# Kernel tuning notes

Hardware: AMD Instinct MI355X
Metric: run time of the kernel (lower is better)

Reference implementation:

```python
import jax, jax.numpy as jnp
import numpy as np
from functools import partial

# Block hyperparams (match init_kwargs)
B, C, N, H = 16, 512, 1024, 8
HID = 4 * C
TAU, THRESH, SG_SCALE = 2.0, 1.0, 5.0
ATTN_SCALE = 0.25
BN_EPS = 1e-5

# LIF spiking neuron (single-step, stateless): membrane v = x / tau, hard threshold
# forward; sigmoid surrogate gradient (scale=5.0) in backward.
@partial(jax.custom_vjp, nondiff_argnums=(1,))
def spike(u, scale):
    return (u >= 0.0).astype(u.dtype)

def _spike_fwd(u, scale):
    return spike(u, scale), u

def _spike_bwd(scale, u, g):
    s = jax.nn.sigmoid(scale * u)
    return (g * scale * s * (1.0 - s),)

spike.defvjp(_spike_fwd, _spike_bwd)

def lif(x):
    return spike(x / TAU - THRESH, SG_SCALE)

def conv1x1(x, w, b=None):
    # x: [B,C,N], w: [O,C] -> [B,O,N]
    y = jnp.einsum('oc,bcn->bon', w, x)
    return y if b is None else y + b[None, :, None]

def bn(x, g, b):
    # BatchNorm1d, training-mode batch stats over (batch, length), biased var
    m = jnp.mean(x, axis=(0, 2), keepdims=True)
    v = jnp.var(x, axis=(0, 2), keepdims=True)
    return (x - m) * jax.lax.rsqrt(v + BN_EPS) * g[None, :, None] + b[None, :, None]


def setup_inputs() -> dict:
    key = jax.random.key(0)
    ks = jax.random.split(key, 8)
    w = lambda k, o, i: jax.random.normal(k, (o, i), dtype=jnp.float32) * 0.02
    inp = {
        'x': jax.random.normal(ks[0], (B, C, N), dtype=jnp.float32),
        'q_w': w(ks[1], C, C), 'q_g': jnp.ones((C,), jnp.float32), 'q_b': jnp.zeros((C,), jnp.float32),
        'k_w': w(ks[2], C, C), 'k_g': jnp.ones((C,), jnp.float32), 'k_b': jnp.zeros((C,), jnp.float32),
        'v_w': w(ks[3], C, C), 'v_g': jnp.ones((C,), jnp.float32), 'v_b': jnp.zeros((C,), jnp.float32),
        'proj_w': w(ks[4], C, C), 'proj_bias': jnp.zeros((C,), jnp.float32),
        'proj_g': jnp.ones((C,), jnp.float32), 'proj_b': jnp.zeros((C,), jnp.float32),
        'fc1_w': w(ks[5], HID, C), 'fc1_bias': jnp.zeros((HID,), jnp.float32),
        'fc1_g': jnp.ones((HID,), jnp.float32), 'fc1_b': jnp.zeros((HID,), jnp.float32),
        'fc2_w': w(ks[6], C, HID), 'fc2_bias': jnp.zeros((C,), jnp.float32),
        'fc2_g': jnp.ones((C,), jnp.float32), 'fc2_b': jnp.zeros((C,), jnp.float32),
    }
    return inp


def reference(x, q_w, q_g, q_b, k_w, k_g, k_b, v_w, v_g, v_b,
              proj_w, proj_bias, proj_g, proj_b,
              fc1_w, fc1_bias, fc1_g, fc1_b, fc2_w, fc2_bias, fc2_g, fc2_b):
    Bb, Cc, Nn = x.shape
    D = Cc // H

    def heads(t):  # [B,C,N] -> [B,H,N,D]
        return t.transpose(0, 2, 1).reshape(Bb, Nn, H, D).transpose(0, 2, 1, 3)

    # spiking attention (no softmax): (Q K^T) V * 0.25
    q = heads(lif(bn(conv1x1(x, q_w), q_g, q_b)))
    k = heads(lif(bn(conv1x1(x, k_w), k_g, k_b)))
    v = heads(lif(bn(conv1x1(x, v_w), v_g, v_b)))
    scores = jnp.einsum('bhnd,bhmd->bhnm', q, k)            # [B,H,N,N]
    attn = jnp.einsum('bhnm,bhmd->bhnd', scores, v) * ATTN_SCALE
    a = attn.transpose(0, 1, 3, 2).reshape(Bb, Cc, Nn)       # [B,C,N]
    a = lif(a)
    a = lif(bn(conv1x1(a, proj_w, proj_bias), proj_g, proj_b))
    x = x + a                                                # residual 1

    # conv1x1-BN-LIF MLP
    h = lif(bn(conv1x1(x, fc1_w, fc1_bias), fc1_g, fc1_b))
    h = lif(bn(conv1x1(h, fc2_w, fc2_bias), fc2_g, fc2_b))
    return x + h                                             # residual 2
```

## Files before the change

kernel.cpp:

```cpp
#include <hip/hip_runtime.h>
#include <stdint.h>

#pragma clang fp contract(off)

#define BATCH 16
#define CCH   512
#define NLEN  1024
#define NH    8
#define DH    64

__device__ float pw128(const float* __restrict__ x) {
    float r0=x[0],r1=x[1],r2=x[2],r3=x[3],r4=x[4],r5=x[5],r6=x[6],r7=x[7];
    for (int i = 8; i < 128; i += 8) {
        r0 += x[i+0]; r1 += x[i+1]; r2 += x[i+2]; r3 += x[i+3];
        r4 += x[i+4]; r5 += x[i+5]; r6 += x[i+6]; r7 += x[i+7];
    }
    return ((r0+r1)+(r2+r3))+((r4+r5)+(r6+r7));
}
__device__ float pw128_sqdev(const float* __restrict__ x, float m) {
    float r0,r1,r2,r3,r4,r5,r6,r7;
    {
        float d;
        d = x[0]-m; r0 = d*d;  d = x[1]-m; r1 = d*d;
        d = x[2]-m; r2 = d*d;  d = x[3]-m; r3 = d*d;
        d = x[4]-m; r4 = d*d;  d = x[5]-m; r5 = d*d;
        d = x[6]-m; r6 = d*d;  d = x[7]-m; r7 = d*d;
    }
    for (int i = 8; i < 128; i += 8) {
        float d;
        d = x[i+0]-m; r0 += d*d;  d = x[i+1]-m; r1 += d*d;
        d = x[i+2]-m; r2 += d*d;  d = x[i+3]-m; r3 += d*d;
        d = x[i+4]-m; r4 += d*d;  d = x[i+5]-m; r5 += d*d;
        d = x[i+6]-m; r6 += d*d;  d = x[i+7]-m; r7 += d*d;
    }
    return ((r0+r1)+(r2+r3))+((r4+r5)+(r6+r7));
}

__global__ __launch_bounds__(64) void bn_stats_np_k(const float* __restrict__ Y, int O,
                                                    float2* __restrict__ st)
{
    const int o = blockIdx.x;
    const int t = threadIdx.x;
    const int bi = t >> 2, q = t & 3;
    __shared__ float part[64];
    __shared__ float msh;
    const float* p = Y + ((size_t)bi * O + o) * NLEN + q * 256;
    {
        float s0 = pw128(p), s1 = pw128(p + 128);
        part[t] = s0 + s1;
    }
    __syncthreads();
    if (t == 0) {
        float s = 0.0f;
        for (int b = 0; b < 16; ++b) {
            const float* pp = &part[b * 4];
            float v = (pp[0] + pp[1]) + (pp[2] + pp[3]);
            s = (b == 0) ? v : (s + v);
        }
        msh = s / 16384.0f;
    }
    __syncthreads();
    const float m = msh;
    {
        float s0 = pw128_sqdev(p, m), s1 = pw128_sqdev(p + 128, m);
        part[t] = s0 + s1;
    }
    __syncthreads();
    if (t == 0) {
        float s = 0.0f;
        for (int b = 0; b < 16; ++b) {
            const float* pp = &part[b * 4];
            float v = (pp[0] + pp[1]) + (pp[2] + pp[3]);
            s = (b == 0) ? v : (s + v);
        }
        float var = s / 16384.0f;
        float ve  = var + 1e-5f;
        float sq  = (float)sqrt((double)ve);
        float r   = (float)(1.0 / (double)sq);
        st[o] = make_float2(m, r);
    }
}

__device__ inline bool spike_f32(float y, float2 s, float g, float b) {
    float t1 = y - s.x;
    float t2 = t1 * s.y;
    float t3 = t2 * g;
    float t4 = t3 + b;
    float u  = t4 / 2.0f - 1.0f;
    return u >= 0.0f;
}

template<int MODE>
__global__ __launch_bounds__(256) void gemm_k(
    const float* __restrict__ W, const float* __restrict__ Xf, const uint8_t* __restrict__ Xs8,
    const float* __restrict__ bias, float* __restrict__ Y,
    int O, int Cin, int N)
{
    __shared__ float Ws[2][16][132];
    __shared__ float Xs[2][16][132];
    const int b = blockIdx.z;
    const size_t xbase = (size_t)b * Cin * N;
    float* Yb = Y + (size_t)b * O * N;
    const int o0 = blockIdx.y * 128;
    const int n0 = blockIdx.x * 128;
    const int t  = threadIdx.x;
    const int tx = t & 15;
    const int ty = t >> 4;

    const int wr = t >> 1;
    const int wk = (t & 1) << 3;
    const int xk = t >> 4;
    const int xc = (t & 15) << 3;

    float acc[8][8];
#pragma unroll
    for (int i = 0; i < 8; ++i)
#pragma unroll
        for (int j = 0; j < 8; ++j) acc[i][j] = 0.0f;

    float4 wA[2];
    float  xr[8];

    auto loadG = [&](int k0) {
        const float* wp = W + (size_t)(o0 + wr) * Cin + k0 + wk;
        wA[0] = *reinterpret_cast<const float4*>(wp);
        wA[1] = *reinterpret_cast<const float4*>(wp + 4);
        size_t off = xbase + (size_t)(k0 + xk) * N + n0 + xc;
        float4 v0 = *reinterpret_cast<const float4*>(Xf + off);
        float4 v1 = *reinterpret_cast<const float4*>(Xf + off + 4);
        if (MODE == 0) {
            xr[0]=v0.x; xr[1]=v0.y; xr[2]=v0.z; xr[3]=v0.w;
            xr[4]=v1.x; xr[5]=v1.y; xr[6]=v1.z; xr[7]=v1.w;
        } else {
            uchar4 u0 = *reinterpret_cast<const uchar4*>(Xs8 + off);
            uchar4 u1 = *reinterpret_cast<const uchar4*>(Xs8 + off + 4);
            xr[0]=v0.x+(float)u0.x; xr[1]=v0.y+(float)u0.y;
            xr[2]=v0.z+(float)u0.z; xr[3]=v0.w+(float)u0.w;
            xr[4]=v1.x+(float)u1.x; xr[5]=v1.y+(float)u1.y;
            xr[6]=v1.z+(float)u1.z; xr[7]=v1.w+(float)u1.w;
        }
    };
    auto stage = [&](int buf) {
        Ws[buf][wk+0][wr]=wA[0].x; Ws[buf][wk+1][wr]=wA[0].y;
        Ws[buf][wk+2][wr]=wA[0].z; Ws[buf][wk+3][wr]=wA[0].w;
        Ws[buf][wk+4][wr]=wA[1].x; Ws[buf][wk+5][wr]=wA[1].y;
        Ws[buf][wk+6][wr]=wA[1].z; Ws[buf][wk+7][wr]=wA[1].w;
        *reinterpret_cast<float4*>(&Xs[buf][xk][xc])     = make_float4(xr[0],xr[1],xr[2],xr[3]);
        *reinterpret_cast<float4*>(&Xs[buf][xk][xc + 4]) = make_float4(xr[4],xr[5],xr[6],xr[7]);
    };

    loadG(0);
    stage(0);
    __syncthreads();
    int cur = 0;
    for (int k0 = 0;;) {
        const int kn = k0 + 16;
        const bool more = kn < Cin;
        if (more) loadG(kn);
#pragma unroll
        for (int kk = 0; kk < 16; ++kk) {
            float4 a0 = *reinterpret_cast<const float4*>(&Ws[cur][kk][ty * 4]);
            float4 a1 = *reinterpret_cast<const float4*>(&Ws[cur][kk][64 + ty * 4]);
            float4 b0 = *reinterpret_cast<const float4*>(&Xs[cur][kk][tx * 4]);
            float4 b1 = *reinterpret_cast<const float4*>(&Xs[cur][kk][64 + tx * 4]);
            float av[8] = {a0.x,a0.y,a0.z,a0.w,a1.x,a1.y,a1.z,a1.w};
            float bv[8] = {b0.x,b0.y,b0.z,b0.w,b1.x,b1.y,b1.z,b1.w};
#pragma unroll
            for (int i = 0; i < 8; ++i)
#pragma unroll
                for (int j = 0; j < 8; ++j)
                    acc[i][j] = fmaf(av[i], bv[j], acc[i][j]);
        }
        if (!more) break;
        stage(cur ^ 1);
        __syncthreads();
        cur ^= 1;
        k0 = kn;
    }
#pragma unroll
    for (int half = 0; half < 2; ++half)
#pragma unroll
        for (int i = 0; i < 4; ++i) {
            const int r = half * 4 + i;
            const int o = o0 + half * 64 + ty * 4 + i;
            const float bb = bias ? bias[o] : 0.0f;
            float* yp = Yb + (size_t)o * N + n0;
            float4 r0, r1;
            r0.x = acc[r][0] + bb; r0.y = acc[r][1] + bb;
            r0.z = acc[r][2] + bb; r0.w = acc[r][3] + bb;
            r1.x = acc[r][4] + bb; r1.y = acc[r][5] + bb;
            r1.z = acc[r][6] + bb; r1.w = acc[r][7] + bb;
            *reinterpret_cast<float4*>(yp + tx * 4)      = r0;
            *reinterpret_cast<float4*>(yp + 64 + tx * 4) = r1;
        }
}

__global__ __launch_bounds__(256) void wt_k(const float* __restrict__ W, float* __restrict__ Wt,
                                            int O, int Cin)
{
    __shared__ float tile[32][33];
    const int k0 = blockIdx.x * 32, o0 = blockIdx.y * 32;
    const int tx = threadIdx.x & 31, ty = threadIdx.x >> 5;
#pragma unroll
    for (int j = 0; j < 4; ++j)
        tile[ty + 8*j][tx] = W[(size_t)(o0 + ty + 8*j) * Cin + k0 + tx];
    __syncthreads();
#pragma unroll
    for (int j = 0; j < 4; ++j)
        Wt[(size_t)(k0 + ty + 8*j) * O + o0 + tx] = tile[tx][ty + 8*j];
}

__global__ __launch_bounds__(256) void col_bits_k(const uint8_t* __restrict__ S,
                                                  unsigned long long* __restrict__ bits, int Cin)
{
    const int n0 = blockIdx.x * 64, kw = blockIdx.y, b = blockIdx.z;
    __shared__ uint8_t tile[64][64];
    const int t = threadIdx.x;
    const int r = t >> 2, cg = (t & 3) * 16;
    const uint8_t* src = S + ((size_t)b * Cin + kw * 64 + r) * NLEN + n0 + cg;
    *reinterpret_cast<uint4*>(&tile[r][cg]) = *reinterpret_cast<const uint4*>(src);
    __syncthreads();
    if (t < 64) {
        unsigned long long m = 0;
#pragma unroll
        for (int rr = 0; rr < 64; ++rr)
            m |= ((unsigned long long)(tile[rr][t] != 0)) << rr;
        bits[((size_t)b * NLEN + n0 + t) * (Cin >> 6) + kw] = m;
    }
}

__global__ __launch_bounds__(256) void sparse_gemm_k(
    const float* __restrict__ Wt, const unsigned long long* __restrict__ bits,
    const float* __restrict__ bias, float* __restrict__ Y, int Cin)
{
    const int wid  = (blockIdx.x << 2) + (threadIdx.x >> 6);
    const int lane = threadIdx.x & 63;
    const int b = wid >> 10, n = wid & 1023;
    const int W64 = Cin >> 6;
    float acc[8];
#pragma unroll
    for (int i = 0; i < 8; ++i) acc[i] = 0.0f;
    const unsigned long long* bp = bits + ((size_t)b * NLEN + n) * W64;
    for (int w = 0; w < W64; ++w) {
        unsigned long long m = bp[w];
        while (m) {
            const int bit = __builtin_ctzll(m);
            m &= m - 1;
            const int k = (w << 6) + bit;
            const float* wr = Wt + ((size_t)k << 9) + lane * 8;
            float4 w0 = *reinterpret_cast<const float4*>(wr);
            float4 w1 = *reinterpret_cast<const float4*>(wr + 4);
            acc[0] += w0.x; acc[1] += w0.y; acc[2] += w0.z; acc[3] += w0.w;
            acc[4] += w1.x; acc[5] += w1.y; acc[6] += w1.z; acc[7] += w1.w;
        }
    }
    const float* bq = bias + lane * 8;
    float4 b0 = *reinterpret_cast<const float4*>(bq);
    float4 b1 = *reinterpret_cast<const float4*>(bq + 4);
    float bi[8] = {b0.x, b0.y, b0.z, b0.w, b1.x, b1.y, b1.z, b1.w};
    float* yp = Y + ((size_t)b * 512 + lane * 8) * NLEN + n;
#pragma unroll
    for (int i = 0; i < 8; ++i)
        yp[(size_t)i * NLEN] = acc[i] + bi[i];
}

__global__ __launch_bounds__(256) void spike_pack_qkv_k(
    const float* __restrict__ Y, const float2* __restrict__ st,
    const float* __restrict__ gq, const float* __restrict__ gk, const float* __restrict__ gv,
    const float* __restrict__ bq, const float* __restrict__ bk, const float* __restrict__ bv,
    uint8_t* __restrict__ oq, uint8_t* __restrict__ ok, uint8_t* __restrict__ ov)
{
    const int nt = blockIdx.x, hs = blockIdx.y, b = blockIdx.z;
    const int tensor = hs >> 3, h = hs & 7;
    const float* g  = (tensor == 0) ? gq : (tensor == 1) ? gk : gv;
    const float* be = (tensor == 0) ? bq : (tensor == 1) ? bk : bv;
    uint8_t* outp   = (tensor == 0) ? oq : (tensor == 1) ? ok : ov;
    __shared__ uint8_t tile[64][68];
    const int t = threadIdx.x;
    {
        const int i = t & 63, dq = t >> 6;
#pragma unroll
        for (int p = 0; p < 16; ++p) {
            int d  = dq * 16 + p;
            int cf = hs * 64 + d;
            int cl = h * 64 + d;
            float y = Y[((size_t)b * 1536 + cf) * NLEN + nt * 64 + i];
            tile[d][i] = spike_f32(y, st[cf], g[cl], be[cl]) ? 1 : 0;
        }
    }
    __syncthreads();
    {
        const int d = t & 63, iq = t >> 6;
#pragma unroll
        for (int p = 0; p < 16; ++p) {
            int i = iq * 16 + p;
            outp[((size_t)(b * NH + h) * NLEN + nt * 64 + i) * DH + d] = tile[d][i];
        }
    }
}

__global__ __launch_bounds__(256) void ktv_k(const uint8_t* __restrict__ Kb, const uint8_t* __restrict__ Vb,
                                             float* __restrict__ M)
{
    const int bh = blockIdx.x;
    const uint8_t* kp = Kb + (size_t)bh * NLEN * DH;
    const uint8_t* vp = Vb + (size_t)bh * NLEN * DH;
    __shared__ float ks[64][68];
    __shared__ float vs[64][68];
    const int t = threadIdx.x;
    const int d2 = t & 63, g4 = t >> 6;
    float acc[16];
#pragma unroll
    for (int j = 0; j < 16; ++j) acc[j] = 0.f;

    for (int nc = 0; nc < NLEN; nc += 64) {
#pragma unroll
        for (int p = 0; p < 16; ++p) {
            int idx = t + p * 256;
            int r = idx >> 6, d = idx & 63;
            ks[r][d] = (float)kp[(size_t)(nc + r) * DH + d];
            vs[r][d] = (float)vp[(size_t)(nc + r) * DH + d];
        }
        __syncthreads();
        for (int n = 0; n < 64; ++n) {
            float vv = vs[n][d2];
#pragma unroll
            for (int j = 0; j < 16; ++j)
                acc[j] += ks[n][g4 * 16 + j] * vv;
        }
        __syncthreads();
    }
#pragma unroll
    for (int j = 0; j < 16; ++j)
        M[(size_t)bh * 4096 + (size_t)(g4 * 16 + j) * 64 + d2] = acc[j];
}

__global__ __launch_bounds__(256) void attn_spike_k(const uint8_t* __restrict__ Qb, const float* __restrict__ M,
                                                    uint8_t* __restrict__ A)
{
    const int nt = blockIdx.x, h = blockIdx.y, b = blockIdx.z;
    const int bh = b * NH + h;
    __shared__ float Ms[64][68];
    __shared__ float qs[64][65];
    const int t = threadIdx.x;
#pragma unroll
    for (int p = 0; p < 16; ++p) {
        int idx = t + p * 256;
        int r = idx >> 6, c = idx & 63;
        Ms[r][c] = M[(size_t)bh * 4096 + idx];
        qs[c][r] = (float)Qb[((size_t)bh * NLEN + nt * 64 + r) * DH + c];
    }
    __syncthreads();
    const int n = t & 63, dg = t >> 6;
    float acc[16];
#pragma unroll
    for (int j = 0; j < 16; ++j) acc[j] = 0.f;
    for (int d1 = 0; d1 < 64; ++d1) {
        float qv = qs[d1][n];
#pragma unroll
        for (int j = 0; j < 16; ++j)
            acc[j] += qv * Ms[d1][dg * 16 + j];
    }
#pragma unroll
    for (int j = 0; j < 16; ++j) {
        int d = dg * 16 + j;
        A[((size_t)b * CCH + h * 64 + d) * NLEN + nt * 64 + n] = (acc[j] >= 8.0f) ? 1 : 0;
    }
}

__global__ __launch_bounds__(256) void spike_store_k(
    const float* __restrict__ Y, const float2* __restrict__ st,
    const float* __restrict__ g, const float* __restrict__ bet,
    uint8_t* __restrict__ H, int Oc, int o_off, int Otot)
{
    size_t i4 = (size_t)blockIdx.x * 256 + threadIdx.x;
    size_t total = (size_t)BATCH * Oc * (NLEN / 4);
    if (i4 >= total) return;
    int n4 = (int)(i4 & 255);
    int o  = (int)((i4 >> 8) % Oc);
    int b  = (int)(i4 / ((size_t)256 * Oc));
    float4 y = reinterpret_cast<const float4*>(Y)[i4];
    float2 s = st[o];
    float gg = g[o], bb = bet[o];
    uchar4 r;
    r.x = spike_f32(y.x, s, gg, bb) ? 1 : 0;
    r.y = spike_f32(y.y, s, gg, bb) ? 1 : 0;
    r.z = spike_f32(y.z, s, gg, bb) ? 1 : 0;
    r.w = spike_f32(y.w, s, gg, bb) ? 1 : 0;
    *reinterpret_cast<uchar4*>(H + ((size_t)(b * Otot + o_off + o)) * NLEN + n4 * 4) = r;
}

__global__ __launch_bounds__(256) void final_k(
    const float* __restrict__ Y, const float2* __restrict__ st,
    const float* __restrict__ g, const float* __restrict__ bet,
    const float* __restrict__ x, const uint8_t* __restrict__ ares,
    float* __restrict__ Out)
{
    size_t i4 = (size_t)blockIdx.x * 256 + threadIdx.x;
    size_t total = (size_t)BATCH * CCH * (NLEN / 4);
    if (i4 >= total) return;
    int o = (int)((i4 >> 8) % CCH);
    float4 y  = reinterpret_cast<const float4*>(Y)[i4];
    float4 xv = reinterpret_cast<const float4*>(x)[i4];
    uchar4 av = reinterpret_cast<const uchar4*>(ares)[i4];
    float2 s = st[o];
    float gg = g[o], bb = bet[o];
    float4 r;
    {
        float x1;
        x1 = xv.x + (float)av.x; r.x = x1 + (spike_f32(y.x, s, gg, bb) ? 1.0f : 0.0f);
        x1 = xv.y + (float)av.y; r.y = x1 + (spike_f32(y.y, s, gg, bb) ? 1.0f : 0.0f);
        x1 = xv.z + (float)av.z; r.z = x1 + (spike_f32(y.z, s, gg, bb) ? 1.0f : 0.0f);
        x1 = xv.w + (float)av.w; r.w = x1 + (spike_f32(y.w, s, gg, bb) ? 1.0f : 0.0f);
    }
    reinterpret_cast<float4*>(Out)[i4] = r;
}

extern "C" void kernel_launch(void* const* d_in, const int* in_sizes, int n_in,
                              void* d_out, int out_size, void* d_ws, size_t ws_size,
                              hipStream_t stream)
{
    const float* x         = (const float*)d_in[0];
    const float* q_w       = (const float*)d_in[1];
    const float* q_g       = (const float*)d_in[2];
    const float* q_b       = (const float*)d_in[3];
    const float* k_w       = (const float*)d_in[4];
    const float* k_g       = (const float*)d_in[5];
    const float* k_b       = (const float*)d_in[6];
    const float* v_w       = (const float*)d_in[7];
    const float* v_g       = (const float*)d_in[8];
    const float* v_b       = (const float*)d_in[9];
    const float* proj_w    = (const float*)d_in[10];
    const float* proj_bias = (const float*)d_in[11];
    const float* proj_g    = (const float*)d_in[12];
    const float* proj_b    = (const float*)d_in[13];
    const float* fc1_w     = (const float*)d_in[14];
    const float* fc1_bias  = (const float*)d_in[15];
    const float* fc1_g     = (const float*)d_in[16];
    const float* fc1_b     = (const float*)d_in[17];
    const float* fc2_w     = (const float*)d_in[18];
    const float* fc2_bias  = (const float*)d_in[19];
    const float* fc2_g     = (const float*)d_in[20];
    const float* fc2_b     = (const float*)d_in[21];
    float* out = (float*)d_out;

    char* ws = (char*)d_ws;
    const size_t MiB = 1ull << 20;
    if (ws_size < 124 * MiB) return;

    float*    Yq    = (float*)(ws);
    float*    Af    = (float*)(ws);
    uint8_t*  ab    = (uint8_t*)(ws);
    uint8_t*  ares  = (uint8_t*)(ws + 64 * MiB);
    uint8_t*  hb    = (uint8_t*)(ws + 72 * MiB);
    uint8_t*  qb    = (uint8_t*)(ws + 96 * MiB);
    uint8_t*  kb    = (uint8_t*)(ws + 104 * MiB);
    uint8_t*  vb    = (uint8_t*)(ws + 112 * MiB);
    float*    Wt    = (float*)(ws + 104 * MiB);
    unsigned long long* bits = (unsigned long long*)(ws + 108 * MiB);
    float*    Wcat  = (float*)(ws + 120 * MiB);
    float*    Mbuf  = (float*)(ws + 120 * MiB);
    float2*   stats = (float2*)(ws + 123 * MiB);

    dim3 thr256(256);

    hipMemcpyAsync(Wcat,          q_w, (size_t)512 * 512 * 4, hipMemcpyDeviceToDevice, stream);
    hipMemcpyAsync(Wcat + 262144, k_w, (size_t)512 * 512 * 4, hipMemcpyDeviceToDevice, stream);
    hipMemcpyAsync(Wcat + 524288, v_w, (size_t)512 * 512 * 4, hipMemcpyDeviceToDevice, stream);
    gemm_k<0><<<dim3(8, 12, 16), thr256, 0, stream>>>(Wcat, x, nullptr, nullptr, Yq, 1536, 512, 1024);
    bn_stats_np_k<<<dim3(1536), dim3(64), 0, stream>>>(Yq, 1536, stats);
    spike_pack_qkv_k<<<dim3(16, 24, 16), thr256, 0, stream>>>(Yq, stats, q_g, k_g, v_g,
                                                              q_b, k_b, v_b, qb, kb, vb);

    ktv_k<<<dim3(128), thr256, 0, stream>>>(kb, vb, Mbuf);
    attn_spike_k<<<dim3(16, 8, 16), thr256, 0, stream>>>(qb, Mbuf, ab);

    wt_k<<<dim3(16, 16), thr256, 0, stream>>>(proj_w, Wt, 512, 512);
    col_bits_k<<<dim3(16, 8, 16), thr256, 0, stream>>>(ab, bits, 512);
    sparse_gemm_k<<<dim3(4096), thr256, 0, stream>>>(Wt, bits, proj_bias, Af, 512);
    bn_stats_np_k<<<dim3(512), dim3(64), 0, stream>>>(Af, 512, stats);
    spike_store_k<<<dim3(8192), thr256, 0, stream>>>(Af, stats, proj_g, proj_b, ares, 512, 0, 512);

    for (int ch = 0; ch < 2; ++ch) {
        gemm_k<2><<<dim3(8, 8, 16), thr256, 0, stream>>>(fc1_w + (size_t)ch * 1024 * 512, x, ares,
                                                         fc1_bias + ch * 1024, Af, 1024, 512, 1024);
        bn_stats_np_k<<<dim3(1024), dim3(64), 0, stream>>>(Af, 1024, stats);
        spike_store_k<<<dim3(16384), thr256, 0, stream>>>(Af, stats, fc1_g + ch * 1024, fc1_b + ch * 1024,
                                                          hb, 1024, ch * 1024, 2048);
    }

    wt_k<<<dim3(64, 16), thr256, 0, stream>>>(fc2_w, Wt, 512, 2048);
    col_bits_k<<<dim3(16, 32, 16), thr256, 0, stream>>>(hb, bits, 2048);
    sparse_gemm_k<<<dim3(4096), thr256, 0, stream>>>(Wt, bits, fc2_bias, Af, 2048);
    bn_stats_np_k<<<dim3(512), dim3(64), 0, stream>>>(Af, 512, stats);
    final_k<<<dim3(8192), thr256, 0, stream>>>(Af, stats, fc2_g, fc2_b, x, ares, out);
}
```

Baseline: 1.450 ms.

## Split KtV across chunks, widen BN stats blocks, drop weight concat copies

The K^T V product is split into 8 sequence chunks per (batch, head) with a separate reduction kernel, which raises block count from 128 to 1024. BN statistics now use 128 threads per channel with a two-level shared reduction. The QKV GEMM picks its weight pointer per block instead of needing three device-to-device copies into a concatenated buffer. The spike-pack output stores and the attention/KtV shared-memory loads are vectorised. The costs are an extra partial-sum buffer and an extra launch, and the BN reduction order changes slightly.

```diff
diff --git a/kernel.cpp b/kernel.cpp
--- a/kernel.cpp
+++ b/kernel.cpp
@@ -36,24 +36,24 @@
     return ((r0+r1)+(r2+r3))+((r4+r5)+(r6+r7));
 }
 
-__global__ __launch_bounds__(64) void bn_stats_np_k(const float* __restrict__ Y, int O,
-                                                    float2* __restrict__ st)
+__global__ __launch_bounds__(128) void bn_stats_np_k(const float* __restrict__ Y, int O,
+                                                     float2* __restrict__ st)
 {
     const int o = blockIdx.x;
     const int t = threadIdx.x;
-    const int bi = t >> 2, q = t & 3;
-    __shared__ float part[64];
+    const int bi = t >> 3, h = t & 7;
+    __shared__ float part[128];
+    __shared__ float sq[64];
     __shared__ float msh;
-    const float* p = Y + ((size_t)bi * O + o) * NLEN + q * 256;
-    {
-        float s0 = pw128(p), s1 = pw128(p + 128);
-        part[t] = s0 + s1;
-    }
+    const float* p = Y + ((size_t)bi * O + o) * NLEN + h * 128;
+    part[t] = pw128(p);
+    __syncthreads();
+    if (t < 64) sq[t] = part[2 * t] + part[2 * t + 1];
     __syncthreads();
     if (t == 0) {
         float s = 0.0f;
         for (int b = 0; b < 16; ++b) {
-            const float* pp = &part[b * 4];
+            const float* pp = &sq[b * 4];
             float v = (pp[0] + pp[1]) + (pp[2] + pp[3]);
             s = (b == 0) ? v : (s + v);
         }
@@ -61,22 +61,21 @@
     }
     __syncthreads();
     const float m = msh;
-    {
-        float s0 = pw128_sqdev(p, m), s1 = pw128_sqdev(p + 128, m);
-        part[t] = s0 + s1;
-    }
+    part[t] = pw128_sqdev(p, m);
+    __syncthreads();
+    if (t < 64) sq[t] = part[2 * t] + part[2 * t + 1];
     __syncthreads();
     if (t == 0) {
         float s = 0.0f;
         for (int b = 0; b < 16; ++b) {
-            const float* pp = &part[b * 4];
+            const float* pp = &sq[b * 4];
             float v = (pp[0] + pp[1]) + (pp[2] + pp[3]);
             s = (b == 0) ? v : (s + v);
         }
         float var = s / 16384.0f;
         float ve  = var + 1e-5f;
-        float sq  = (float)sqrt((double)ve);
-        float r   = (float)(1.0 / (double)sq);
+        float sqv = (float)sqrt((double)ve);
+        float r   = (float)(1.0 / (double)sqv);
         st[o] = make_float2(m, r);
     }
 }
@@ -92,7 +91,8 @@
 
 template<int MODE>
 __global__ __launch_bounds__(256) void gemm_k(
-    const float* __restrict__ W, const float* __restrict__ Xf, const uint8_t* __restrict__ Xs8,
+    const float* __restrict__ Wq, const float* __restrict__ Wk, const float* __restrict__ Wv,
+    const float* __restrict__ Xf, const uint8_t* __restrict__ Xs8,
     const float* __restrict__ bias, float* __restrict__ Y,
     int O, int Cin, int N)
 {
@@ -101,7 +101,17 @@
     const int b = blockIdx.z;
     const size_t xbase = (size_t)b * Cin * N;
     float* Yb = Y + (size_t)b * O * N;
-    const int o0 = blockIdx.y * 128;
+    const int oy  = blockIdx.y;
+    const int o0y = oy * 128;
+    const float* W;
+    int o0w;
+    if (MODE == 0) {
+        W   = (oy < 4) ? Wq : (oy < 8) ? Wk : Wv;
+        o0w = (oy & 3) * 128;
+    } else {
+        W   = Wq;
+        o0w = o0y;
+    }
     const int n0 = blockIdx.x * 128;
     const int t  = threadIdx.x;
     const int tx = t & 15;
@@ -122,7 +132,7 @@
     float  xr[8];
 
     auto loadG = [&](int k0) {
-        const float* wp = W + (size_t)(o0 + wr) * Cin + k0 + wk;
+        const float* wp = W + (size_t)(o0w + wr) * Cin + k0 + wk;
         wA[0] = *reinterpret_cast<const float4*>(wp);
         wA[1] = *reinterpret_cast<const float4*>(wp + 4);
         size_t off = xbase + (size_t)(k0 + xk) * N + n0 + xc;
@@ -182,7 +192,7 @@
 #pragma unroll
         for (int i = 0; i < 4; ++i) {
             const int r = half * 4 + i;
-            const int o = o0 + half * 64 + ty * 4 + i;
+            const int o = o0y + half * 64 + ty * 4 + i;
             const float bb = bias ? bias[o] : 0.0f;
             float* yp = Yb + (size_t)o * N + n0;
             float4 r0, r1;
@@ -196,7 +206,7 @@
 }
 
 __global__ __launch_bounds__(256) void wt_k(const float* __restrict__ W, float* __restrict__ Wt,
-                                            int O, int Cin)
+                                            int O, int Cin, int o_off, int Otot)
 {
     __shared__ float tile[32][33];
     const int k0 = blockIdx.x * 32, o0 = blockIdx.y * 32;
@@ -207,7 +217,7 @@
     __syncthreads();
 #pragma unroll
     for (int j = 0; j < 4; ++j)
-        Wt[(size_t)(k0 + ty + 8*j) * O + o0 + tx] = tile[tx][ty + 8*j];
+        Wt[(size_t)(k0 + ty + 8*j) * Otot + o_off + o0 + tx] = tile[tx][ty + 8*j];
 }
 
 __global__ __launch_bounds__(256) void col_bits_k(const uint8_t* __restrict__ S,
@@ -290,49 +300,80 @@
     }
     __syncthreads();
     {
-        const int d = t & 63, iq = t >> 6;
-#pragma unroll
-        for (int p = 0; p < 16; ++p) {
-            int i = iq * 16 + p;
-            outp[((size_t)(b * NH + h) * NLEN + nt * 64 + i) * DH + d] = tile[d][i];
-        }
-    }
-}
-
-__global__ __launch_bounds__(256) void ktv_k(const uint8_t* __restrict__ Kb, const uint8_t* __restrict__ Vb,
-                                             float* __restrict__ M)
-{
-    const int bh = blockIdx.x;
+        const int d4 = (t & 15) * 4, ig = t >> 4;
+        uint8_t* ob = outp + ((size_t)(b * NH + h) * NLEN + nt * 64) * DH;
+#pragma unroll
+        for (int p = 0; p < 4; ++p) {
+            int i = p * 16 + ig;
+            uchar4 v;
+            v.x = tile[d4 + 0][i]; v.y = tile[d4 + 1][i];
+            v.z = tile[d4 + 2][i]; v.w = tile[d4 + 3][i];
+            *reinterpret_cast<uchar4*>(ob + (size_t)i * DH + d4) = v;
+        }
+    }
+}
+
+__global__ __launch_bounds__(256) void ktv_part_k(const uint8_t* __restrict__ Kb,
+                                                  const uint8_t* __restrict__ Vb,
+                                                  float* __restrict__ Mp)
+{
+    const int bh = blockIdx.x, ch = blockIdx.y;
     const uint8_t* kp = Kb + (size_t)bh * NLEN * DH;
     const uint8_t* vp = Vb + (size_t)bh * NLEN * DH;
     __shared__ float ks[64][68];
     __shared__ float vs[64][68];
     const int t = threadIdx.x;
     const int d2 = t & 63, g4 = t >> 6;
+    const int r2 = t >> 2, dq = (t & 3) * 16;
     float acc[16];
 #pragma unroll
     for (int j = 0; j < 16; ++j) acc[j] = 0.f;
 
-    for (int nc = 0; nc < NLEN; nc += 64) {
-#pragma unroll
-        for (int p = 0; p < 16; ++p) {
-            int idx = t + p * 256;
-            int r = idx >> 6, d = idx & 63;
-            ks[r][d] = (float)kp[(size_t)(nc + r) * DH + d];
-            vs[r][d] = (float)vp[(size_t)(nc + r) * DH + d];
+    for (int nc = ch * 128; nc < ch * 128 + 128; nc += 64) {
+        uint4 kv = *reinterpret_cast<const uint4*>(kp + (size_t)(nc + r2) * DH + dq);
+        uint4 vv = *reinterpret_cast<const uint4*>(vp + (size_t)(nc + r2) * DH + dq);
+        const uint8_t* k8 = reinterpret_cast<const uint8_t*>(&kv);
+        const uint8_t* v8 = reinterpret_cast<const uint8_t*>(&vv);
+#pragma unroll
+        for (int j = 0; j < 16; j += 4) {
+            float4 kf, vf;
+            kf.x = (float)k8[j+0]; kf.y = (float)k8[j+1];
+            kf.z = (float)k8[j+2]; kf.w = (float)k8[j+3];
+            vf.x = (float)v8[j+0]; vf.y = (float)v8[j+1];
+            vf.z = (float)v8[j+2]; vf.w = (float)v8[j+3];
+            *reinterpret_cast<float4*>(&ks[r2][dq + j]) = kf;
+            *reinterpret_cast<float4*>(&vs[r2][dq + j]) = vf;
         }
         __syncthreads();
         for (int n = 0; n < 64; ++n) {
-            float vv = vs[n][d2];
+            float vvv = vs[n][d2];
 #pragma unroll
             for (int j = 0; j < 16; ++j)
-                acc[j] += ks[n][g4 * 16 + j] * vv;
+                acc[j] += ks[n][g4 * 16 + j] * vvv;
         }
         __syncthreads();
     }
 #pragma unroll
     for (int j = 0; j < 16; ++j)
-        M[(size_t)bh * 4096 + (size_t)(g4 * 16 + j) * 64 + d2] = acc[j];
+        Mp[((size_t)ch * 128 + bh) * 4096 + (size_t)(g4 * 16 + j) * 64 + d2] = acc[j];
+}
+
+__global__ __launch_bounds__(256) void ktv_reduce_k(const float* __restrict__ Mp,
+                                                    float* __restrict__ M)
+{
+    const int bh = blockIdx.x;
+    const int t = threadIdx.x;
+#pragma unroll
+    for (int j = 0; j < 16; j += 4) {
+        const int idx = t * 16 + j;
+        float4 s = *reinterpret_cast<const float4*>(&Mp[(size_t)bh * 4096 + idx]);
+#pragma unroll
+        for (int c = 1; c < 8; ++c) {
+            float4 v = *reinterpret_cast<const float4*>(&Mp[((size_t)c * 128 + bh) * 4096 + idx]);
+            s.x += v.x; s.y += v.y; s.z += v.z; s.w += v.w;
+        }
+        *reinterpret_cast<float4*>(&M[(size_t)bh * 4096 + idx]) = s;
+    }
 }
 
 __global__ __launch_bounds__(256) void attn_spike_k(const uint8_t* __restrict__ Qb, const float* __restrict__ M,
@@ -343,12 +384,19 @@
     __shared__ float Ms[64][68];
     __shared__ float qs[64][65];
     const int t = threadIdx.x;
-#pragma unroll
-    for (int p = 0; p < 16; ++p) {
-        int idx = t + p * 256;
-        int r = idx >> 6, c = idx & 63;
-        Ms[r][c] = M[(size_t)bh * 4096 + idx];
-        qs[c][r] = (float)Qb[((size_t)bh * NLEN + nt * 64 + r) * DH + c];
+    const int r2 = t >> 2, cq = (t & 3) * 16;
+    {
+        const float* mp = M + (size_t)bh * 4096 + (size_t)r2 * 64 + cq;
+#pragma unroll
+        for (int u = 0; u < 4; ++u)
+            *reinterpret_cast<float4*>(&Ms[r2][cq + 4 * u]) =
+                *reinterpret_cast<const float4*>(mp + 4 * u);
+        uint4 qv = *reinterpret_cast<const uint4*>(
+            Qb + ((size_t)bh * NLEN + nt * 64 + r2) * DH + cq);
+        const uint8_t* q8 = reinterpret_cast<const uint8_t*>(&qv);
+#pragma unroll
+        for (int j = 0; j < 16; ++j)
+            qs[cq + j][r2] = (float)q8[j];
     }
     __syncthreads();
     const int n = t & 63, dg = t >> 6;
@@ -451,6 +499,7 @@
     float*    Yq    = (float*)(ws);
     float*    Af    = (float*)(ws);
     uint8_t*  ab    = (uint8_t*)(ws);
+    float*    Mpart = (float*)(ws + 16 * MiB);
     uint8_t*  ares  = (uint8_t*)(ws + 64 * MiB);
     uint8_t*  hb    = (uint8_t*)(ws + 72 * MiB);
     uint8_t*  qb    = (uint8_t*)(ws + 96 * MiB);
@@ -458,40 +507,40 @@
     uint8_t*  vb    = (uint8_t*)(ws + 112 * MiB);
     float*    Wt    = (float*)(ws + 104 * MiB);
     unsigned long long* bits = (unsigned long long*)(ws + 108 * MiB);
-    float*    Wcat  = (float*)(ws + 120 * MiB);
     float*    Mbuf  = (float*)(ws + 120 * MiB);
     float2*   stats = (float2*)(ws + 123 * MiB);
 
-    dim3 thr256(256);
-
-    hipMemcpyAsync(Wcat,          q_w, (size_t)512 * 512 * 4, hipMemcpyDeviceToDevice, stream);
-    hipMemcpyAsync(Wcat + 262144, k_w, (size_t)512 * 512 * 4, hipMemcpyDeviceToDevice, stream);
-    hipMemcpyAsync(Wcat + 524288, v_w, (size_t)512 * 512 * 4, hipMemcpyDeviceToDevice, stream);
-    gemm_k<0><<<dim3(8, 12, 16), thr256, 0, stream>>>(Wcat, x, nullptr, nullptr, Yq, 1536, 512, 1024);
-    bn_stats_np_k<<<dim3(1536), dim3(64), 0, stream>>>(Yq, 1536, stats);
+    dim3 thr256(256), thr128(128);
+
+    gemm_k<0><<<dim3(8, 12, 16), thr256, 0, stream>>>(q_w, k_w, v_w, x, nullptr, nullptr, Yq,
+                                                      1536, 512, 1024);
+    bn_stats_np_k<<<dim3(1536), thr128, 0, stream>>>(Yq, 1536, stats);
     spike_pack_qkv_k<<<dim3(16, 24, 16), thr256, 0, stream>>>(Yq, stats, q_g, k_g, v_g,
                                                               q_b, k_b, v_b, qb, kb, vb);
 
-    ktv_k<<<dim3(128), thr256, 0, stream>>>(kb, vb, Mbuf);
+    ktv_part_k<<<dim3(128, 8), thr256, 0, stream>>>(kb, vb, Mpart);
+    ktv_reduce_k<<<dim3(128), thr256, 0, stream>>>(Mpart, Mbuf);
     attn_spike_k<<<dim3(16, 8, 16), thr256, 0, stream>>>(qb, Mbuf, ab);
 
-    wt_k<<<dim3(16, 16), thr256, 0, stream>>>(proj_w, Wt, 512, 512);
+    wt_k<<<dim3(16, 16), thr256, 0, stream>>>(proj_w, Wt, 512, 512, 0, 512);
     col_bits_k<<<dim3(16, 8, 16), thr256, 0, stream>>>(ab, bits, 512);
     sparse_gemm_k<<<dim3(4096), thr256, 0, stream>>>(Wt, bits, proj_bias, Af, 512);
-    bn_stats_np_k<<<dim3(512), dim3(64), 0, stream>>>(Af, 512, stats);
+    bn_stats_np_k<<<dim3(512), thr128, 0, stream>>>(Af, 512, stats);
     spike_store_k<<<dim3(8192), thr256, 0, stream>>>(Af, stats, proj_g, proj_b, ares, 512, 0, 512);
 
     for (int ch = 0; ch < 2; ++ch) {
-        gemm_k<2><<<dim3(8, 8, 16), thr256, 0, stream>>>(fc1_w + (size_t)ch * 1024 * 512, x, ares,
-                                                         fc1_bias + ch * 1024, Af, 1024, 512, 1024);
-        bn_stats_np_k<<<dim3(1024), dim3(64), 0, stream>>>(Af, 1024, stats);
+        const float* Wc = fc1_w + (size_t)ch * 1024 * 512;
+        gemm_k<2><<<dim3(8, 8, 16), thr256, 0, stream>>>(Wc, Wc, Wc, x, ares,
+                                                         fc1_bias + ch * 1024, Af,
+                                                         1024, 512, 1024);
+        bn_stats_np_k<<<dim3(1024), thr128, 0, stream>>>(Af, 1024, stats);
         spike_store_k<<<dim3(16384), thr256, 0, stream>>>(Af, stats, fc1_g + ch * 1024, fc1_b + ch * 1024,
                                                           hb, 1024, ch * 1024, 2048);
     }
 
-    wt_k<<<dim3(64, 16), thr256, 0, stream>>>(fc2_w, Wt, 512, 2048);
+    wt_k<<<dim3(64, 16), thr256, 0, stream>>>(fc2_w, Wt, 512, 2048, 0, 512);
     col_bits_k<<<dim3(16, 32, 16), thr256, 0, stream>>>(hb, bits, 2048);
     sparse_gemm_k<<<dim3(4096), thr256, 0, stream>>>(Wt, bits, fc2_bias, Af, 2048);
-    bn_stats_np_k<<<dim3(512), dim3(64), 0, stream>>>(Af, 512, stats);
+    bn_stats_np_k<<<dim3(512), thr128, 0, stream>>>(Af, 512, stats);
     final_k<<<dim3(8192), thr256, 0, stream>>>(Af, stats, fc2_g, fc2_b, x, ares, out);
 }
```

Result: faster. 1.316 ms (-9.3%).
